# Performance work log

Measured on AMD Instinct MI355X. Metric: run time of the kernel, lower is better.

Reference implementation:

```python
import jax, jax.numpy as jnp
import numpy as np

DT = 0.1  # Euler timestep (init kwarg)

def setup_inputs() -> dict:
    key = jax.random.key(0)
    ks = jax.random.split(key, 6)
    B, L, S, U, H = 1024, 512, 64, 32, 512
    return {
        "initial_state": jax.random.normal(ks[0], (B, S), dtype=jnp.float32),
        "control_inputs": jax.random.normal(ks[1], (B, L, U), dtype=jnp.float32),
        "W1": jax.random.normal(ks[2], (S + U, H), dtype=jnp.float32) * (1.0 / np.sqrt(S + U)),
        "b1": jnp.zeros((H,), dtype=jnp.float32),
        "W2": jax.random.normal(ks[3], (H, S), dtype=jnp.float32) * (1.0 / np.sqrt(H)),
        "b2": jnp.zeros((S,), dtype=jnp.float32),
    }

def reference(initial_state, control_inputs, W1, b1, W2, b2):
    # Euler integration: state_{t+1} = state_t + dt * f(state_t, u_t)
    # f is a 2-layer tanh MLP on the concatenated [state, control].
    def step(state, u):
        z = jnp.concatenate([state, u], axis=-1)        # (B, S+U)
        diff = jnp.tanh(z @ W1 + b1) @ W2 + b2          # (B, S)
        new_state = state + diff * DT
        return new_state, new_state

    u_seq = jnp.swapaxes(control_inputs, 0, 1)          # (L, B, U)
    _, states = jax.lax.scan(step, initial_state, u_seq)  # (L, B, S)
    return jnp.swapaxes(states, 0, 1)                   # (B, L, S)
```

## Files before the change

kernel.cpp:

```cpp
#include <hip/hip_runtime.h>
#include <hip/hip_fp16.h>


typedef _Float16 f16;
typedef __attribute__((ext_vector_type(8))) _Float16 f16x8;
typedef __attribute__((ext_vector_type(4))) float f32x4;

#define MFMA16(a, b, c) __builtin_amdgcn_mfma_f32_16x16x32_f16((a), (b), (c), 0, 0, 0)

__device__ __forceinline__ float tanh_fast(float x) {
    float t = __builtin_amdgcn_exp2f(x * 2.885390081777927f);
    float r = __builtin_amdgcn_rcpf(t + 1.0f);
    return __builtin_fmaf(-2.0f, r, 1.0f);
}

__global__ __launch_bounds__(512, 2)
void euler_kernel(const float* __restrict__ init,
                  const float* __restrict__ uin,
                  const float* __restrict__ W1,
                  const float* __restrict__ b1,
                  const float* __restrict__ W2,
                  const float* __restrict__ b2,
                  float* __restrict__ out) {
    const int L = 512, S = 64, U = 32, H = 512;
    const int tid  = threadIdx.x;
    const int lane = tid & 63;
    const int w    = tid >> 6;
    const int g    = lane >> 4;
    const int r16  = lane & 15;
    const int ks   = w >> 2;
    const int ns   = w & 3;
    const int ncol0 = w * 64;
    const int b0   = blockIdx.x * 16;

    __shared__ f16  zbuf[16][200];
    __shared__ f16  hbuf[16][520];
    __shared__ float redbuf[4][256];

    f16x8 W1F[6][4];
    #pragma unroll
    for (int kk = 0; kk < 6; ++kk)
      #pragma unroll
      for (int nf = 0; nf < 4; ++nf)
        #pragma unroll
        for (int j = 0; j < 8; ++j) {
            int k  = kk * 32 + g * 8 + j;
            int kr = (k < 128) ? (k & 63) : (64 + (k & 31));
            W1F[kk][nf][j] = (f16)W1[kr * H + ncol0 + nf * 16 + r16];
        }
    f16x8 W2F[8];
    #pragma unroll
    for (int kk = 0; kk < 8; ++kk)
      #pragma unroll
      for (int j = 0; j < 8; ++j) {
          int k = ks * 256 + kk * 32 + g * 8 + j;
          W2F[kk][j] = (f16)W2[k * S + ns * 16 + r16];
      }
    float b1v[4];
    #pragma unroll
    for (int nf = 0; nf < 4; ++nf) b1v[nf] = b1[ncol0 + nf * 16 + r16];
    const float b2v = b2[ns * 16 + r16];

    float stateF[4] = {0.f, 0.f, 0.f, 0.f};
    float ua = 0.f, ub = 0.f;
    int urow = 0, ucol = 0;
    if (ks == 0) {
        #pragma unroll
        for (int j = 0; j < 4; ++j) {
            float s = init[(size_t)(b0 + g * 4 + j) * S + ns * 16 + r16];
            stateF[j] = s;
            f16 sh = (f16)s;
            zbuf[g * 4 + j][ns * 16 + r16]      = sh;
            zbuf[g * 4 + j][64 + ns * 16 + r16] = (f16)(s - (float)sh);
        }
    } else {
        urow = ns * 4 + (lane >> 4);
        ucol = 2 * (lane & 15);
        const float* up = uin + (size_t)(b0 + urow) * L * U + ucol;
        float a = up[0], b = up[1];
        f16 ah = (f16)a, bh = (f16)b;
        zbuf[urow][128 + ucol]     = ah;
        zbuf[urow][128 + ucol + 1] = bh;
        zbuf[urow][160 + ucol]     = (f16)(a - (float)ah);
        zbuf[urow][160 + ucol + 1] = (f16)(b - (float)bh);
        ua = up[U]; ub = up[U + 1];
    }
    __syncthreads();

    #pragma unroll 1
    for (int t = 0; t < L; ++t) {
        f16x8 zf[6];
        #pragma unroll
        for (int kk = 0; kk < 6; ++kk)
            zf[kk] = *(const f16x8*)&zbuf[r16][kk * 32 + g * 8];
        f32x4 acc1[4];
        #pragma unroll
        for (int nf = 0; nf < 4; ++nf)
            acc1[nf] = (f32x4){b1v[nf], b1v[nf], b1v[nf], b1v[nf]};
        #pragma unroll
        for (int kk = 0; kk < 6; ++kk)
          #pragma unroll
          for (int nf = 0; nf < 4; ++nf)
            acc1[nf] = MFMA16(zf[kk], W1F[kk][nf], acc1[nf]);
        #pragma unroll
        for (int nf = 0; nf < 4; ++nf)
          #pragma unroll
          for (int j = 0; j < 4; ++j)
            hbuf[g * 4 + j][ncol0 + nf * 16 + r16] = (f16)tanh_fast(acc1[nf][j]);
        __syncthreads();

        f32x4 acc2 = (f32x4){0.f, 0.f, 0.f, 0.f};
        #pragma unroll
        for (int kk = 0; kk < 8; ++kk) {
            f16x8 hf = *(const f16x8*)&hbuf[r16][ks * 256 + kk * 32 + g * 8];
            acc2 = MFMA16(hf, W2F[kk], acc2);
        }
        if (ks == 1) {
            *(f32x4*)&redbuf[ns][lane * 4] = acc2;
            if (t + 1 < L) {
                f16 ah = (f16)ua, bh = (f16)ub;
                zbuf[urow][128 + ucol]     = ah;
                zbuf[urow][128 + ucol + 1] = bh;
                zbuf[urow][160 + ucol]     = (f16)(ua - (float)ah);
                zbuf[urow][160 + ucol + 1] = (f16)(ub - (float)bh);
            }
            if (t + 2 < L) {
                const float* up = uin + (size_t)(b0 + urow) * L * U + (size_t)(t + 2) * U + ucol;
                ua = up[0]; ub = up[1];
            }
        }
        __syncthreads();

        if (ks == 0) {
            const f32x4 part = *(const f32x4*)&redbuf[ns][lane * 4];
            #pragma unroll
            for (int j = 0; j < 4; ++j) {
                float d = acc2[j] + part[j] + b2v;
                float s = __builtin_fmaf(0.1f, d, stateF[j]);
                stateF[j] = s;
                out[((size_t)(b0 + g * 4 + j) * L + t) * S + ns * 16 + r16] = s;
                f16 sh = (f16)s;
                zbuf[g * 4 + j][ns * 16 + r16]      = sh;
                zbuf[g * 4 + j][64 + ns * 16 + r16] = (f16)(s - (float)sh);
            }
        }
        __syncthreads();
    }
}

extern "C" void kernel_launch(void* const* d_in, const int* in_sizes, int n_in,
                              void* d_out, int out_size, void* d_ws, size_t ws_size,
                              hipStream_t stream) {
    const float* init = (const float*)d_in[0];
    const float* uin  = (const float*)d_in[1];
    const float* W1   = (const float*)d_in[2];
    const float* b1   = (const float*)d_in[3];
    const float* W2   = (const float*)d_in[4];
    const float* b2   = (const float*)d_in[5];
    euler_kernel<<<dim3(64), dim3(512), 0, stream>>>(init, uin, W1, b1, W2, b2,
                                                     (float*)d_out);
}
```

Measured before the change: 719.5 us.

## Drop split-K reduction barrier by giving four waves full-K second layer

```diff
diff --git a/kernel.cpp b/kernel.cpp
--- a/kernel.cpp
+++ b/kernel.cpp
@@ -3,6 +3,7 @@
 
 
 typedef _Float16 f16;
+typedef __attribute__((ext_vector_type(4))) _Float16 f16x4;
 typedef __attribute__((ext_vector_type(8))) _Float16 f16x8;
 typedef __attribute__((ext_vector_type(4))) float f32x4;
 
@@ -28,14 +29,10 @@
     const int w    = tid >> 6;
     const int g    = lane >> 4;
     const int r16  = lane & 15;
-    const int ks   = w >> 2;
-    const int ns   = w & 3;
-    const int ncol0 = w * 64;
     const int b0   = blockIdx.x * 16;
 
-    __shared__ f16  zbuf[16][200];
-    __shared__ f16  hbuf[16][520];
-    __shared__ float redbuf[4][256];
+    __shared__ f16 zbuf[16][200];
+    __shared__ f16 hbuf[16][520];
 
     f16x8 W1F[6][4];
     #pragma unroll
@@ -46,44 +43,49 @@
         for (int j = 0; j < 8; ++j) {
             int k  = kk * 32 + g * 8 + j;
             int kr = (k < 128) ? (k & 63) : (64 + (k & 31));
-            W1F[kk][nf][j] = (f16)W1[kr * H + ncol0 + nf * 16 + r16];
+            W1F[kk][nf][j] = (f16)W1[kr * H + w * 64 + nf * 16 + r16];
         }
-    f16x8 W2F[8];
+    f32x4 b1v[4];
     #pragma unroll
-    for (int kk = 0; kk < 8; ++kk)
-      #pragma unroll
-      for (int j = 0; j < 8; ++j) {
-          int k = ks * 256 + kk * 32 + g * 8 + j;
-          W2F[kk][j] = (f16)W2[k * S + ns * 16 + r16];
-      }
-    float b1v[4];
-    #pragma unroll
-    for (int nf = 0; nf < 4; ++nf) b1v[nf] = b1[ncol0 + nf * 16 + r16];
-    const float b2v = b2[ns * 16 + r16];
+    for (int nf = 0; nf < 4; ++nf)
+        b1v[nf] = *(const f32x4*)&b1[w * 64 + nf * 16 + g * 4];
 
-    float stateF[4] = {0.f, 0.f, 0.f, 0.f};
-    float ua = 0.f, ub = 0.f;
-    int urow = 0, ucol = 0;
-    if (ks == 0) {
+    f16x8 W2F[16];
+    f32x4 b2v = (f32x4){0.f, 0.f, 0.f, 0.f};
+    f32x4 stateF = (f32x4){0.f, 0.f, 0.f, 0.f};
+    f32x4 ua0 = (f32x4){0.f, 0.f, 0.f, 0.f}, ua1 = ua0;
+    if (w < 4) {
+        #pragma unroll
+        for (int kk = 0; kk < 16; ++kk)
+          #pragma unroll
+          for (int j = 0; j < 8; ++j) {
+              int k = kk * 32 + g * 8 + j;
+              W2F[kk][j] = (f16)W2[k * S + w * 16 + r16];
+          }
+        b2v = *(const f32x4*)&b2[w * 16 + g * 4];
+        stateF = *(const f32x4*)&init[(size_t)(b0 + r16) * S + w * 16 + g * 4];
+        f16x4 sh, sl;
         #pragma unroll
         for (int j = 0; j < 4; ++j) {
-            float s = init[(size_t)(b0 + g * 4 + j) * S + ns * 16 + r16];
-            stateF[j] = s;
-            f16 sh = (f16)s;
-            zbuf[g * 4 + j][ns * 16 + r16]      = sh;
-            zbuf[g * 4 + j][64 + ns * 16 + r16] = (f16)(s - (float)sh);
+            sh[j] = (f16)stateF[j];
+            sl[j] = (f16)(stateF[j] - (float)sh[j]);
         }
+        *(f16x4*)&zbuf[r16][w * 16 + g * 4]      = sh;
+        *(f16x4*)&zbuf[r16][64 + w * 16 + g * 4] = sl;
     } else {
-        urow = ns * 4 + (lane >> 4);
-        ucol = 2 * (lane & 15);
-        const float* up = uin + (size_t)(b0 + urow) * L * U + ucol;
-        float a = up[0], b = up[1];
-        f16 ah = (f16)a, bh = (f16)b;
-        zbuf[urow][128 + ucol]     = ah;
-        zbuf[urow][128 + ucol + 1] = bh;
-        zbuf[urow][160 + ucol]     = (f16)(a - (float)ah);
-        zbuf[urow][160 + ucol + 1] = (f16)(b - (float)bh);
-        ua = up[U]; ub = up[U + 1];
+        const float* up = uin + (size_t)(b0 + r16) * L * U + g * 8;
+        f32x4 u0 = *(const f32x4*)up;
+        f32x4 u1 = *(const f32x4*)(up + 4);
+        f16x8 uh, ul;
+        #pragma unroll
+        for (int j = 0; j < 4; ++j) {
+            f16 h0 = (f16)u0[j]; uh[j] = h0;     ul[j] = (f16)(u0[j] - (float)h0);
+            f16 h1 = (f16)u1[j]; uh[4 + j] = h1; ul[4 + j] = (f16)(u1[j] - (float)h1);
+        }
+        *(f16x8*)&zbuf[r16][128 + g * 8] = uh;
+        *(f16x8*)&zbuf[r16][160 + g * 8] = ul;
+        ua0 = *(const f32x4*)(up + U);
+        ua1 = *(const f32x4*)(up + U + 4);
     }
     __syncthreads();
 
@@ -95,53 +97,61 @@
             zf[kk] = *(const f16x8*)&zbuf[r16][kk * 32 + g * 8];
         f32x4 acc1[4];
         #pragma unroll
-        for (int nf = 0; nf < 4; ++nf)
-            acc1[nf] = (f32x4){b1v[nf], b1v[nf], b1v[nf], b1v[nf]};
+        for (int nf = 0; nf < 4; ++nf) acc1[nf] = b1v[nf];
         #pragma unroll
         for (int kk = 0; kk < 6; ++kk)
           #pragma unroll
           for (int nf = 0; nf < 4; ++nf)
-            acc1[nf] = MFMA16(zf[kk], W1F[kk][nf], acc1[nf]);
+            acc1[nf] = MFMA16(W1F[kk][nf], zf[kk], acc1[nf]);
         #pragma unroll
-        for (int nf = 0; nf < 4; ++nf)
-          #pragma unroll
-          for (int j = 0; j < 4; ++j)
-            hbuf[g * 4 + j][ncol0 + nf * 16 + r16] = (f16)tanh_fast(acc1[nf][j]);
-        __syncthreads();
-
-        f32x4 acc2 = (f32x4){0.f, 0.f, 0.f, 0.f};
-        #pragma unroll
-        for (int kk = 0; kk < 8; ++kk) {
-            f16x8 hf = *(const f16x8*)&hbuf[r16][ks * 256 + kk * 32 + g * 8];
-            acc2 = MFMA16(hf, W2F[kk], acc2);
-        }
-        if (ks == 1) {
-            *(f32x4*)&redbuf[ns][lane * 4] = acc2;
-            if (t + 1 < L) {
-                f16 ah = (f16)ua, bh = (f16)ub;
-                zbuf[urow][128 + ucol]     = ah;
-                zbuf[urow][128 + ucol + 1] = bh;
-                zbuf[urow][160 + ucol]     = (f16)(ua - (float)ah);
-                zbuf[urow][160 + ucol + 1] = (f16)(ub - (float)bh);
-            }
-            if (t + 2 < L) {
-                const float* up = uin + (size_t)(b0 + urow) * L * U + (size_t)(t + 2) * U + ucol;
-                ua = up[0]; ub = up[1];
-            }
+        for (int nf = 0; nf < 4; ++nf) {
+            f16x4 hv;
+            #pragma unroll
+            for (int j = 0; j < 4; ++j) hv[j] = (f16)tanh_fast(acc1[nf][j]);
+            *(f16x4*)&hbuf[r16][w * 64 + nf * 16 + g * 4] = hv;
         }
         __syncthreads();
 
-        if (ks == 0) {
-            const f32x4 part = *(const f32x4*)&redbuf[ns][lane * 4];
+        if (w < 4) {
+            f32x4 accA = (f32x4){0.f, 0.f, 0.f, 0.f};
+            f32x4 accB = (f32x4){0.f, 0.f, 0.f, 0.f};
+            #pragma unroll
+            for (int kk = 0; kk < 8; ++kk) {
+                f16x8 hf = *(const f16x8*)&hbuf[r16][kk * 32 + g * 8];
+                accA = MFMA16(W2F[kk], hf, accA);
+            }
+            #pragma unroll
+            for (int kk = 8; kk < 16; ++kk) {
+                f16x8 hf = *(const f16x8*)&hbuf[r16][kk * 32 + g * 8];
+                accB = MFMA16(W2F[kk], hf, accB);
+            }
+            f16x4 sh, sl;
             #pragma unroll
             for (int j = 0; j < 4; ++j) {
-                float d = acc2[j] + part[j] + b2v;
+                float d = (accA[j] + accB[j]) + b2v[j];
                 float s = __builtin_fmaf(0.1f, d, stateF[j]);
                 stateF[j] = s;
-                out[((size_t)(b0 + g * 4 + j) * L + t) * S + ns * 16 + r16] = s;
-                f16 sh = (f16)s;
-                zbuf[g * 4 + j][ns * 16 + r16]      = sh;
-                zbuf[g * 4 + j][64 + ns * 16 + r16] = (f16)(s - (float)sh);
+                sh[j] = (f16)s;
+                sl[j] = (f16)(s - (float)sh[j]);
+            }
+            *(f32x4*)&out[((size_t)(b0 + r16) * L + t) * S + w * 16 + g * 4] = stateF;
+            *(f16x4*)&zbuf[r16][w * 16 + g * 4]      = sh;
+            *(f16x4*)&zbuf[r16][64 + w * 16 + g * 4] = sl;
+        } else {
+            if (t + 1 < L) {
+                f16x8 uh, ul;
+                #pragma unroll
+                for (int j = 0; j < 4; ++j) {
+                    f16 h0 = (f16)ua0[j]; uh[j] = h0;     ul[j] = (f16)(ua0[j] - (float)h0);
+                    f16 h1 = (f16)ua1[j]; uh[4 + j] = h1; ul[4 + j] = (f16)(ua1[j] - (float)h1);
+                }
+                *(f16x8*)&zbuf[r16][128 + g * 8] = uh;
+                *(f16x8*)&zbuf[r16][160 + g * 8] = ul;
+            }
+            if (t + 2 < L) {
+                const float* up = uin + (size_t)(b0 + r16) * L * U + (size_t)(t + 2) * U + g * 8;
+                ua0 = *(const f32x4*)up;
+                ua1 = *(const f32x4*)(up + 4);
             }
         }
         __syncthreads();
```

Result: faster. 664.7 us (-7.6%).
